# Performance work log

Measured on AMD Instinct MI355X. Metric: run time of the kernel, lower is better.

## Reference

```python
import jax, jax.numpy as jnp
import numpy as np

N = 50000
E = 800000
IN_F = 256
OUT_F = 64
NHEAD = 4
ALPHA = 0.2  # LeakyReLU negative slope


def setup_inputs() -> dict:
    key = jax.random.key(0)
    k1, k2, k3, k4, k5 = jax.random.split(key, 5)
    x = jax.random.normal(k1, (N, IN_F), dtype=jnp.float32)
    edge = jax.random.randint(k2, (2, E), 0, N, dtype=jnp.int32)
    # params init ~ uniform(-stdv, stdv), stdv = sqrt(6/(fan_in+fan_out))
    stdv_W = float(np.sqrt(6.0 / (IN_F + OUT_F * NHEAD)))
    W = jax.random.uniform(k3, (IN_F, OUT_F * NHEAD), jnp.float32, -stdv_W, stdv_W)
    stdv_a = float(np.sqrt(6.0 / (NHEAD + OUT_F)))
    a_l = jax.random.uniform(k4, (1, NHEAD, OUT_F), jnp.float32, -stdv_a, stdv_a)
    a_r = jax.random.uniform(k5, (1, NHEAD, OUT_F), jnp.float32, -stdv_a, stdv_a)
    return {"x": x, "edge": edge, "W": W, "a_l": a_l, "a_r": a_r}


def _gat_forward(x, W, a_l, a_r, edge):
    n = x.shape[0]
    row, col = edge[0], edge[1]
    # dense projection: [N, IN_F] @ [IN_F, NHEAD*OUT_F] -> [N, NHEAD, OUT_F]
    h = (x @ W).reshape(n, NHEAD, OUT_F)
    # per-node, per-head attention logits
    hl = jnp.sum(a_l * h, axis=-1)  # [N, NHEAD]
    hr = jnp.sum(a_r * h, axis=-1)  # [N, NHEAD]
    # per-edge score, LeakyReLU
    e = jax.nn.leaky_relu(hl[row] + hr[col], negative_slope=ALPHA)  # [E, NHEAD]
    # segment softmax over edges grouped by destination row (per head)
    e_max = jax.ops.segment_max(e, row, num_segments=n)  # [N, NHEAD]
    e_max = jnp.where(jnp.isfinite(e_max), e_max, 0.0)   # empty segments -> -inf
    ee = jnp.exp(e - e_max[row])
    denom = jax.ops.segment_sum(ee, row, num_segments=n)  # [N, NHEAD]
    att = ee / denom[row]  # [E, NHEAD]; dropout is identity in eval mode
    # spmm aggregation: out[row] += att * h[col]   -> [N, NHEAD, OUT_F]
    msg = att[:, :, None] * h[col]
    out_h = jax.ops.segment_sum(msg, row, num_segments=n)
    # concat heads
    return out_h.reshape(n, NHEAD * OUT_F)


def reference(x, edge, W, a_l, a_r):
    return _gat_forward(x, W, a_l, a_r, edge)
```

## Files before the change

kernel.cpp:

```cpp
#include <hip/hip_runtime.h>
#include <math.h>

#define NN 50000
#define NE 800000
#define KDIM 256
#define CDIM 256
#define NHEAD 4
#define HF 64
#define ALPHA 0.2f
#define RCAP 64

typedef short bh8 __attribute__((ext_vector_type(8)));
typedef float f32x4 __attribute__((ext_vector_type(4)));


__device__ __forceinline__ unsigned short f2bf(float f) {
  unsigned u = __float_as_uint(f);
  return (unsigned short)((u + 0x7FFFu + ((u >> 16) & 1u)) >> 16);
}
__device__ __forceinline__ float bf2f(unsigned short u) {
  return __uint_as_float((unsigned)u << 16);
}
__device__ __forceinline__ float4 bf4_to_f4(ushort4 u) {
  float4 r;
  r.x = bf2f(u.x); r.y = bf2f(u.y); r.z = bf2f(u.z); r.w = bf2f(u.w);
  return r;
}

__device__ __forceinline__ void wcvt_one(const float* __restrict__ W, int i,
                                         unsigned short* __restrict__ wt_hi,
                                         unsigned short* __restrict__ wt_lo) {
  int gcol = i & 255, k = i >> 8;
  int nb = gcol >> 7, col = gcol & 127, kt = k >> 5, kk = k & 31;
  float v = W[(size_t)k * CDIM + gcol];
  unsigned short hi = f2bf(v);
  int dst = (nb * 8 + kt) * 4096 + col * 32 + kk;
  wt_hi[dst] = hi;
  wt_lo[dst] = f2bf(v - bf2f(hi));
}

__global__ __launch_bounds__(256) void append_csr(const int* __restrict__ edge,
                                                  int* __restrict__ deg,
                                                  int* __restrict__ colpad,
                                                  const float* __restrict__ W,
                                                  unsigned short* __restrict__ wt_hi,
                                                  unsigned short* __restrict__ wt_lo) {
  int e = blockIdx.x * 256 + threadIdx.x;
  if (e < NE) {
    int r = edge[e], c = edge[NE + e];
    int pos = atomicAdd(&deg[r], 1);
    colpad[(r << 6) + min(pos, RCAP - 1)] = c;
  }
  if (e < KDIM * CDIM) wcvt_one(W, e, wt_hi, wt_lo);
}

#define LDS_AHI 0
#define LDS_ALO 2560
#define LDS_BHI 5120
#define LDS_BLO 10240
#define LDS_TOT 15360

__global__ __launch_bounds__(256, 2) void gemm_fused(const float* __restrict__ X,
                                                     const unsigned short* __restrict__ wt_hi,
                                                     const unsigned short* __restrict__ wt_lo,
                                                     const float* __restrict__ al,
                                                     const float* __restrict__ ar,
                                                     unsigned short* __restrict__ hb,
                                                     float* __restrict__ hl,
                                                     float* __restrict__ hr, int M) {
  __shared__ unsigned short lds[LDS_TOT];
  const int tid = threadIdx.x;
  const int lane = tid & 63;
  const int wid = tid >> 6;
  const int wm = wid >> 1, wn = wid & 1;
  const int nb = blockIdx.x;
  const int row0 = blockIdx.y * 64;
  const int frow = lane & 15;
  const int fk = (lane >> 4) * 8;
  const int arow = tid >> 2;
  const int akc = (tid & 3) * 8;
  const int hd = nb * 2 + wn;

  f32x4 acc[2][4] = {};

  for (int kt = 0; kt < 8; ++kt) {
    float4 a0 = make_float4(0.f, 0.f, 0.f, 0.f), a1 = a0;
    {
      int gr = row0 + arow;
      if (gr < M) {
        const float* p = &X[(size_t)gr * KDIM + kt * 32 + akc];
        a0 = *(const float4*)p;
        a1 = *(const float4*)(p + 4);
      }
    }
    const int bbase = (nb * 8 + kt) * 4096;
    uint4 b0h = *(const uint4*)&wt_hi[bbase + tid * 8];
    uint4 b1h = *(const uint4*)&wt_hi[bbase + 2048 + tid * 8];
    uint4 b0l = *(const uint4*)&wt_lo[bbase + tid * 8];
    uint4 b1l = *(const uint4*)&wt_lo[bbase + 2048 + tid * 8];
    __syncthreads();
    {
      float va[8] = {a0.x, a0.y, a0.z, a0.w, a1.x, a1.y, a1.z, a1.w};
      bh8 ahi, alo;
#pragma unroll
      for (int j = 0; j < 8; ++j) {
        unsigned short h = f2bf(va[j]);
        ahi[j] = (short)h;
        alo[j] = (short)f2bf(va[j] - bf2f(h));
      }
      *(bh8*)&lds[LDS_AHI + arow * 40 + akc] = ahi;
      *(bh8*)&lds[LDS_ALO + arow * 40 + akc] = alo;
    }
    {
      int f0 = tid * 8, c0 = f0 >> 5, k0 = f0 & 31;
      *(uint4*)&lds[LDS_BHI + c0 * 40 + k0] = b0h;
      *(uint4*)&lds[LDS_BLO + c0 * 40 + k0] = b0l;
      int f1 = 2048 + tid * 8, c1 = f1 >> 5, k1 = f1 & 31;
      *(uint4*)&lds[LDS_BHI + c1 * 40 + k1] = b1h;
      *(uint4*)&lds[LDS_BLO + c1 * 40 + k1] = b1l;
    }
    __syncthreads();
    bh8 fah[2], fal[2];
#pragma unroll
    for (int mi = 0; mi < 2; ++mi) {
      fah[mi] = *(const bh8*)&lds[LDS_AHI + (wm * 32 + mi * 16 + frow) * 40 + fk];
      fal[mi] = *(const bh8*)&lds[LDS_ALO + (wm * 32 + mi * 16 + frow) * 40 + fk];
    }
#pragma unroll
    for (int ni = 0; ni < 4; ++ni) {
      int c = wn * 64 + ni * 16 + frow;
      bh8 fbh = *(const bh8*)&lds[LDS_BHI + c * 40 + fk];
      bh8 fbl = *(const bh8*)&lds[LDS_BLO + c * 40 + fk];
#pragma unroll
      for (int mi = 0; mi < 2; ++mi) {
        acc[mi][ni] = __builtin_amdgcn_mfma_f32_16x16x32_bf16(fah[mi], fbh, acc[mi][ni], 0, 0, 0);
        acc[mi][ni] = __builtin_amdgcn_mfma_f32_16x16x32_bf16(fah[mi], fbl, acc[mi][ni], 0, 0, 0);
        acc[mi][ni] = __builtin_amdgcn_mfma_f32_16x16x32_bf16(fal[mi], fbh, acc[mi][ni], 0, 0, 0);
      }
    }
  }

  float alv[4], arv[4];
#pragma unroll
  for (int ni = 0; ni < 4; ++ni) {
    alv[ni] = al[hd * 64 + ni * 16 + frow];
    arv[ni] = ar[hd * 64 + ni * 16 + frow];
  }
#pragma unroll
  for (int mi = 0; mi < 2; ++mi) {
#pragma unroll
    for (int rg = 0; rg < 4; ++rg) {
      float sl = 0.f, sr = 0.f;
#pragma unroll
      for (int ni = 0; ni < 4; ++ni) {
        float cv = acc[mi][ni][rg];
        sl += cv * alv[ni];
        sr += cv * arv[ni];
      }
#pragma unroll
      for (int off = 1; off < 16; off <<= 1) {
        sl += __shfl_xor(sl, off);
        sr += __shfl_xor(sr, off);
      }
      int r = row0 + wm * 32 + mi * 16 + (lane >> 4) * 4 + rg;
      if ((lane & 15) == 0 && r < M) {
        hl[(size_t)r * 4 + hd] = sl;
        hr[(size_t)r * 4 + hd] = sr;
      }
    }
  }

  __syncthreads();
  const int cbase = wid * 2304;
#pragma unroll
  for (int mi = 0; mi < 2; ++mi)
#pragma unroll
    for (int ni = 0; ni < 4; ++ni)
#pragma unroll
      for (int rg = 0; rg < 4; ++rg)
        lds[cbase + (mi * 16 + (lane >> 4) * 4 + rg) * 72 + ni * 16 + frow] =
            f2bf(acc[mi][ni][rg]);
  __syncthreads();
#pragma unroll
  for (int it = 0; it < 4; ++it) {
    int chunk = it * 64 + lane;
    int rr = chunk >> 3, cc = chunk & 7;
    uint4 v = *(const uint4*)&lds[cbase + rr * 72 + cc * 8];
    int grr = row0 + wm * 32 + rr;
    if (grr < M)
      *(uint4*)&hb[(size_t)grr * CDIM + hd * 64 + cc * 8] = v;
  }
}

__global__ __launch_bounds__(256) void row_aggregate(const int* __restrict__ deg,
                                                     const int* __restrict__ colpad,
                                                     const float* __restrict__ hl,
                                                     const float* __restrict__ hr,
                                                     const unsigned short* __restrict__ hb,
                                                     float* __restrict__ out) {
  int row = (int)((blockIdx.x * 256 + threadIdx.x) >> 6);
  int lane = threadIdx.x & 63;
  if (row >= NN) return;
  int n = min(deg[row], RCAP);
  int head = lane >> 4;
  int f8 = lane * 4;
  float hlv = hl[row * 4 + head];
  float4 acc = make_float4(0.f, 0.f, 0.f, 0.f);
  float den = 0.f;

  if (n > 0) {
    int myc = colpad[(row << 6) + min(lane, n - 1)];
    ushort4 u0, u1, u2, u3;
    float r0, r1, r2, r3;

#define LDSLOT(S, J)                                                        \
  {                                                                         \
    int cc_ = __shfl(myc, min((J), n - 1));                                 \
    u##S = *(const ushort4*)&hb[cc_ * CDIM + f8];                           \
    r##S = hr[cc_ * 4 + head];                                              \
  }
#define STEP(S)                                                             \
  {                                                                         \
    float sc_ = hlv + r##S;                                                 \
    sc_ = sc_ > 0.f ? sc_ : ALPHA * sc_;                                    \
    float ee_ = __expf(sc_);                                                \
    den += ee_;                                                             \
    float4 hv_ = bf4_to_f4(u##S);                                           \
    acc.x += ee_ * hv_.x; acc.y += ee_ * hv_.y;                             \
    acc.z += ee_ * hv_.z; acc.w += ee_ * hv_.w;                             \
  }

    LDSLOT(0, 0) LDSLOT(1, 1) LDSLOT(2, 2) LDSLOT(3, 3)
    for (int j = 0; j < n; j += 4) {
      STEP(0)
      LDSLOT(0, j + 4)
      if (j + 1 < n) STEP(1)
      LDSLOT(1, j + 5)
      if (j + 2 < n) STEP(2)
      LDSLOT(2, j + 6)
      if (j + 3 < n) STEP(3)
      LDSLOT(3, j + 7)
    }
#undef LDSLOT
#undef STEP
  }

  float rd = den > 0.f ? 1.f / den : 0.f;
  acc.x *= rd; acc.y *= rd; acc.z *= rd; acc.w *= rd;
  *(float4*)&out[row * CDIM + f8] = acc;
}


extern "C" void kernel_launch(void* const* d_in, const int* in_sizes, int n_in,
                              void* d_out, int out_size, void* d_ws, size_t ws_size,
                              hipStream_t stream) {
  const float* x   = (const float*)d_in[0];
  const int*  edge = (const int*)d_in[1];
  const float* W   = (const float*)d_in[2];
  const float* al  = (const float*)d_in[3];
  const float* ar  = (const float*)d_in[4];
  float* out = (float*)d_out;

  char* base = (char*)d_ws;
  unsigned short* hb = (unsigned short*)base;
  float* hl = (float*)(base + (size_t)NN * CDIM * 2);
  float* hr = hl + (size_t)NN * NHEAD;
  unsigned short* wt_hi = (unsigned short*)(hr + (size_t)NN * NHEAD);
  unsigned short* wt_lo = wt_hi + KDIM * CDIM;
  int* deg    = (int*)(wt_lo + KDIM * CDIM);
  int* colpad = deg + NN;

  hipMemsetAsync(deg, 0, (size_t)NN * sizeof(int), stream);

  append_csr<<<(NE + 255) / 256, 256, 0, stream>>>(edge, deg, colpad, W, wt_hi, wt_lo);

  gemm_fused<<<dim3(2, (NN + 63) / 64), 256, 0, stream>>>(x, wt_hi, wt_lo, al, ar, hb, hl, hr, NN);

  row_aggregate<<<(NN * 64 + 255) / 256, 256, 0, stream>>>(deg, colpad, hl, hr, hb, out);
}
```

Baseline: 246.3 us.

## Merge CSR build into GEMM launch and fold memset into W conversion

Replaces the memset plus append_csr plus gemm launches with a small kernel that zeroes deg and converts W, followed by one kernel whose grid holds both the GEMM tiles and the edge-append blocks, so the two independent phases can run concurrently. It also scales hl/hr by log2(e) so the aggregation can use the hardware exp2 instead of __expf. The cost targeted is launch overhead and the serialization between the atomic-bound CSR build and the compute-bound GEMM. In exchange, the heterogeneous blocks may compete for resources, and the append blocks inherit the GEMM kernel's LDS and launch bounds.

```diff
diff --git a/kernel.cpp b/kernel.cpp
--- a/kernel.cpp
+++ b/kernel.cpp
@@ -9,6 +9,10 @@
 #define HF 64
 #define ALPHA 0.2f
 #define RCAP 64
+#define LOG2E 1.44269504088896f
+
+#define GEMM_NBLK (2 * ((NN + 63) / 64))
+#define APPEND_NBLK ((NE + 255) / 256)
 
 typedef short bh8 __attribute__((ext_vector_type(8)));
 typedef float f32x4 __attribute__((ext_vector_type(4)));
@@ -27,9 +31,12 @@
   return r;
 }
 
-__device__ __forceinline__ void wcvt_one(const float* __restrict__ W, int i,
-                                         unsigned short* __restrict__ wt_hi,
-                                         unsigned short* __restrict__ wt_lo) {
+__global__ __launch_bounds__(256) void zero_wcvt(int* __restrict__ deg,
+                                                 const float* __restrict__ W,
+                                                 unsigned short* __restrict__ wt_hi,
+                                                 unsigned short* __restrict__ wt_lo) {
+  int i = blockIdx.x * 256 + threadIdx.x;
+  if (i < NN) deg[i] = 0;
   int gcol = i & 255, k = i >> 8;
   int nb = gcol >> 7, col = gcol & 127, kt = k >> 5, kk = k & 31;
   float v = W[(size_t)k * CDIM + gcol];
@@ -39,42 +46,42 @@
   wt_lo[dst] = f2bf(v - bf2f(hi));
 }
 
-__global__ __launch_bounds__(256) void append_csr(const int* __restrict__ edge,
-                                                  int* __restrict__ deg,
-                                                  int* __restrict__ colpad,
-                                                  const float* __restrict__ W,
-                                                  unsigned short* __restrict__ wt_hi,
-                                                  unsigned short* __restrict__ wt_lo) {
-  int e = blockIdx.x * 256 + threadIdx.x;
-  if (e < NE) {
-    int r = edge[e], c = edge[NE + e];
-    int pos = atomicAdd(&deg[r], 1);
-    colpad[(r << 6) + min(pos, RCAP - 1)] = c;
-  }
-  if (e < KDIM * CDIM) wcvt_one(W, e, wt_hi, wt_lo);
-}
-
 #define LDS_AHI 0
 #define LDS_ALO 2560
 #define LDS_BHI 5120
 #define LDS_BLO 10240
 #define LDS_TOT 15360
 
-__global__ __launch_bounds__(256, 2) void gemm_fused(const float* __restrict__ X,
+__global__ __launch_bounds__(256, 2) void prep_fused(const float* __restrict__ X,
                                                      const unsigned short* __restrict__ wt_hi,
                                                      const unsigned short* __restrict__ wt_lo,
                                                      const float* __restrict__ al,
                                                      const float* __restrict__ ar,
                                                      unsigned short* __restrict__ hb,
                                                      float* __restrict__ hl,
-                                                     float* __restrict__ hr, int M) {
+                                                     float* __restrict__ hr,
+                                                     const int* __restrict__ edge,
+                                                     int* __restrict__ deg,
+                                                     int* __restrict__ colpad, int M) {
   __shared__ unsigned short lds[LDS_TOT];
+  const int bid = blockIdx.x;
   const int tid = threadIdx.x;
+
+  if (bid >= GEMM_NBLK) {
+    int e = (bid - GEMM_NBLK) * 256 + tid;
+    if (e < NE) {
+      int r = edge[e], c = edge[NE + e];
+      int pos = atomicAdd(&deg[r], 1);
+      colpad[(r << 6) + min(pos, RCAP - 1)] = c;
+    }
+    return;
+  }
+
   const int lane = tid & 63;
   const int wid = tid >> 6;
   const int wm = wid >> 1, wn = wid & 1;
-  const int nb = blockIdx.x;
-  const int row0 = blockIdx.y * 64;
+  const int nb = bid & 1;
+  const int row0 = (bid >> 1) * 64;
   const int frow = lane & 15;
   const int fk = (lane >> 4) * 8;
   const int arow = tid >> 2;
@@ -164,8 +171,8 @@
       }
       int r = row0 + wm * 32 + mi * 16 + (lane >> 4) * 4 + rg;
       if ((lane & 15) == 0 && r < M) {
-        hl[(size_t)r * 4 + hd] = sl;
-        hr[(size_t)r * 4 + hd] = sr;
+        hl[(size_t)r * 4 + hd] = sl * LOG2E;
+        hr[(size_t)r * 4 + hd] = sr * LOG2E;
       }
     }
   }
@@ -223,7 +230,7 @@
   {                                                                         \
     float sc_ = hlv + r##S;                                                 \
     sc_ = sc_ > 0.f ? sc_ : ALPHA * sc_;                                    \
-    float ee_ = __expf(sc_);                                                \
+    float ee_ = __builtin_amdgcn_exp2f(sc_);                                \
     den += ee_;                                                             \
     float4 hv_ = bf4_to_f4(u##S);                                           \
     acc.x += ee_ * hv_.x; acc.y += ee_ * hv_.y;                             \
@@ -270,11 +277,10 @@
   int* deg    = (int*)(wt_lo + KDIM * CDIM);
   int* colpad = deg + NN;
 
-  hipMemsetAsync(deg, 0, (size_t)NN * sizeof(int), stream);
-
-  append_csr<<<(NE + 255) / 256, 256, 0, stream>>>(edge, deg, colpad, W, wt_hi, wt_lo);
-
-  gemm_fused<<<dim3(2, (NN + 63) / 64), 256, 0, stream>>>(x, wt_hi, wt_lo, al, ar, hb, hl, hr, NN);
+  zero_wcvt<<<256, 256, 0, stream>>>(deg, W, wt_hi, wt_lo);
+
+  prep_fused<<<GEMM_NBLK + APPEND_NBLK, 256, 0, stream>>>(
+      x, wt_hi, wt_lo, al, ar, hb, hl, hr, edge, deg, colpad, NN);
 
   row_aggregate<<<(NN * 64 + 255) / 256, 256, 0, stream>>>(deg, colpad, hl, hr, hb, out);
 }
```

Result: faster. 229.1 us (-7.0%).
